# Kernel tuning notes

Hardware: AMD Instinct MI355X
Metric: run time of the kernel (lower is better)

The kernel has to match this reference:

```python
import jax, jax.numpy as jnp
import numpy as np

B, S, D = 2, 2048, 2048
H, KVH = 16, 4
HD = D // H  # 128


def _rope_angles(seq, head_dim):
    theta = 1.0 / (10000.0 ** (jnp.arange(0, head_dim, 2, dtype=jnp.float32) / head_dim))
    ang = jnp.arange(seq, dtype=jnp.float32)[:, None] * theta[None, :]  # [S, HD/2]
    return jnp.cos(ang), jnp.sin(ang)


def _apply_rotary(t, cos, sin):
    # t: [B, S, h, HD]; pairs are (even, odd) along last dim (view_as_complex semantics)
    tr = t[..., 0::2]
    ti = t[..., 1::2]
    c = cos[None, :, None, :]
    s = sin[None, :, None, :]
    out_r = tr * c - ti * s
    out_i = tr * s + ti * c
    return jnp.stack([out_r, out_i], axis=-1).reshape(t.shape)


def setup_inputs() -> dict:
    key = jax.random.key(0)
    ks = jax.random.split(key, 8)
    sd = 1.0 / np.sqrt(D)
    return {
        'x': jax.random.normal(ks[0], (B, S, D), dtype=jnp.float32),
        'wq': jax.random.normal(ks[1], (D, D), dtype=jnp.float32) * sd,
        'bq': jax.random.normal(ks[2], (D,), dtype=jnp.float32) * 0.01,
        'wk': jax.random.normal(ks[3], (D, KVH * HD), dtype=jnp.float32) * sd,
        'bk': jax.random.normal(ks[4], (KVH * HD,), dtype=jnp.float32) * 0.01,
        'wv': jax.random.normal(ks[5], (D, KVH * HD), dtype=jnp.float32) * sd,
        'bv': jax.random.normal(ks[6], (KVH * HD,), dtype=jnp.float32) * 0.01,
        'wo': jax.random.normal(ks[7], (D, D), dtype=jnp.float32) * sd,
    }


def reference(x, wq, bq, wk, bk, wv, bv, wo):
    b, s, d = x.shape
    q = (x @ wq + bq).reshape(b, s, H, HD)
    k = (x @ wk + bk).reshape(b, s, KVH, HD)
    v = (x @ wv + bv).reshape(b, s, KVH, HD)

    cos, sin = _rope_angles(s, HD)
    q = _apply_rotary(q, cos, sin)
    k = _apply_rotary(k, cos, sin)

    repeat = H // KVH
    k = jnp.repeat(k, repeat, axis=2)  # [B, S, H, HD]
    v = jnp.repeat(v, repeat, axis=2)

    scale = 1.0 / np.sqrt(HD)
    att_score = jnp.einsum('bqhd,bkhd->bqhk', q, k) * scale  # [B, S, H, S]
    att_weight = jax.nn.softmax(att_score, axis=-1)
    out = jnp.einsum('bqhk,bkhd->bqhd', att_weight, v)
    out = out.reshape(b, s, H * HD)
    return out @ wo
```

## Files before the change

kernel.cpp:

```cpp
#include <hip/hip_runtime.h>
#include <hip/hip_bf16.h>
#include <cstdint>

typedef __attribute__((ext_vector_type(4))) float f32x4;
typedef __attribute__((ext_vector_type(16))) float f32x16;
typedef __attribute__((ext_vector_type(8))) short bf16x8;
typedef __attribute__((ext_vector_type(4))) unsigned int u32x4;
typedef unsigned short u16;
typedef unsigned int u32;

__device__ __forceinline__ u16 f2b(float x) {
  __hip_bfloat16 h = __float2bfloat16(x);
  return *reinterpret_cast<u16*>(&h);
}

__device__ __forceinline__ u32 pk(float a, float b) {
  return ((u32)f2b(b) << 16) | (u32)f2b(a);
}

__device__ __forceinline__ void gload16(const void* g, void* l) {
  __builtin_amdgcn_global_load_lds((const __attribute__((address_space(1))) u32*)g,
                                   (__attribute__((address_space(3))) u32*)l, 16, 0, 0);
}

__device__ __forceinline__ float xmax32(float x) {
  return fmaxf(x, __shfl_xor(x, 32, 64));
}
__device__ __forceinline__ float xsum32(float x) {
  return x + __shfl_xor(x, 32, 64);
}


__global__ void cvt_f32_bf16(const float* __restrict__ in, u16* __restrict__ out, int n4) {
  int idx = (blockIdx.x * 256 + threadIdx.x);
  if (idx < n4) {
    const float4 v = *(const float4*)(in + (size_t)idx * 4);
    u16* o = out + (size_t)idx * 4;
    o[0] = f2b(v.x); o[1] = f2b(v.y); o[2] = f2b(v.z); o[3] = f2b(v.w);
  }
}

__global__ void w_transpose_cvt(const float* __restrict__ w0, const float* __restrict__ w1,
                                const float* __restrict__ w2, int b0, int b1,
                                int N0, int N1, int N2,
                                u16* __restrict__ out, int K) {
  __shared__ float tile[32][33];
  int k0 = blockIdx.x * 32, n0 = blockIdx.y * 32;
  const float* src; int srcN; int c0;
  if (n0 < b0)      { src = w0; srcN = N0; c0 = n0; }
  else if (n0 < b1) { src = w1; srcN = N1; c0 = n0 - b0; }
  else              { src = w2; srcN = N2; c0 = n0 - b1; }
  int tx = threadIdx.x & 31, ty = threadIdx.x >> 5;
#pragma unroll
  for (int j = 0; j < 32; j += 8)
    tile[ty + j][tx] = src[(size_t)(k0 + ty + j) * srcN + c0 + tx];
  __syncthreads();
#pragma unroll
  for (int j = 0; j < 32; j += 8)
    out[(size_t)(n0 + ty + j) * K + k0 + tx] = f2b(tile[tx][ty + j]);
}

__global__ void pack_bias(const float* __restrict__ bq, const float* __restrict__ bk,
                          const float* __restrict__ bv, float* __restrict__ out) {
  int i = blockIdx.x * 256 + threadIdx.x;
  if (i < 3072) out[i] = (i < 2048) ? bq[i] : ((i < 2560) ? bk[i - 2048] : bv[i - 2560]);
}

__global__ void v_transpose_cvt(const float* __restrict__ qkv, u16* __restrict__ vt) {
  __shared__ float tile[32][33];
  int s0 = blockIdx.x * 32;
  int d0 = blockIdx.y * 32;
  int z = blockIdx.z;
  int b = z >> 2, kvh = z & 3;
  int tx = threadIdx.x & 31, ty = threadIdx.x >> 5;
#pragma unroll
  for (int j = 0; j < 32; j += 8)
    tile[ty + j][tx] = qkv[((size_t)(b * 2048 + s0 + ty + j)) * 3072 + 2560 + kvh * 128 + d0 + tx];
  __syncthreads();
#pragma unroll
  for (int j = 0; j < 32; j += 8)
    vt[((size_t)z * 128 + d0 + ty + j) * 2048 + s0 + tx] = f2b(tile[tx][ty + j]);
}

__global__ void rope_cvt(const float* __restrict__ qkv, u16* __restrict__ out,
                         int lognh, int col0, float scale) {
  int idx = blockIdx.x * 256 + threadIdx.x;
  int i = idx & 63;
  int nh = 1 << lognh;
  int h = (idx >> 6) & (nh - 1);
  int bs = idx >> (6 + lognh);
  int s = bs & 2047;
  int b = bs >> 11;
  const float* src = qkv + (size_t)bs * 3072 + col0 + h * 128 + 2 * i;
  float tr = src[0], ti = src[1];
  float theta = expf(-(float)i * 0.14391156831212787f);
  float ang = (float)s * theta;
  float sv, cv;
  sincosf(ang, &sv, &cv);
  float orr = (tr * cv - ti * sv) * scale;
  float oii = (tr * sv + ti * cv) * scale;
  u16* dst = out + (((size_t)(b * nh + h) * 2048 + s) * 128 + 2 * i);
  dst[0] = f2b(orr);
  dst[1] = f2b(oii);
}

__global__ __launch_bounds__(256) void gemm_bt_bf16(
    const u16* __restrict__ A, const u16* __restrict__ Bt,
    const float* __restrict__ bias, float* __restrict__ C,
    int M, int N, int K) {
  __shared__ u16 As[128 * 32];
  __shared__ u16 Bs[128 * 32];
  const int tid = threadIdx.x;
  const int lane = tid & 63;
  const int w = tid >> 6;
  const int wr = w >> 1, wc = w & 1;
  const int m0 = blockIdx.y * 128;
  const int n0 = blockIdx.x * 128;

  f32x4 acc[4][4] = {};

  for (int k0 = 0; k0 < K; k0 += 32) {
#pragma unroll
    for (int it = 0; it < 2; ++it) {
      int c = tid + it * 256;
      int row = c >> 2;
      int off = (c & 3) * 8;
      gload16(A + (size_t)(m0 + row) * K + k0 + off, (u16*)As + w * 512 + it * 2048);
      gload16(Bt + (size_t)(n0 + row) * K + k0 + off, (u16*)Bs + w * 512 + it * 2048);
    }
    __syncthreads();
    const int col8 = (lane >> 4) * 8;
    bf16x8 a[4], bfr[4];
#pragma unroll
    for (int m = 0; m < 4; ++m)
      a[m] = *(const bf16x8*)&As[(wr * 64 + m * 16 + (lane & 15)) * 32 + col8];
#pragma unroll
    for (int n = 0; n < 4; ++n)
      bfr[n] = *(const bf16x8*)&Bs[(wc * 64 + n * 16 + (lane & 15)) * 32 + col8];
#pragma unroll
    for (int m = 0; m < 4; ++m)
#pragma unroll
      for (int n = 0; n < 4; ++n)
        acc[m][n] = __builtin_amdgcn_mfma_f32_16x16x32_bf16(a[m], bfr[n], acc[m][n], 0, 0, 0);
    __syncthreads();
  }

#pragma unroll
  for (int m = 0; m < 4; ++m) {
    int row = m0 + wr * 64 + m * 16 + ((lane >> 4) << 2);
#pragma unroll
    for (int n = 0; n < 4; ++n) {
      int col = n0 + wc * 64 + n * 16 + (lane & 15);
      float bvv = bias ? bias[col] : 0.f;
      float* cp = C + (size_t)row * N + col;
#pragma unroll
      for (int r = 0; r < 4; ++r) cp[(size_t)r * N] = acc[m][n][r] + bvv;
    }
  }
}

__global__ __launch_bounds__(128, 3) void flash_attn(
    const u16* __restrict__ Qr, const u16* __restrict__ Kr,
    const u16* __restrict__ Vt, u16* __restrict__ Att) {
  __shared__ u16 Ks[2][32 * 128];
  __shared__ u16 Vs[2][128 * 32];
  const int tid = threadIdx.x, lane = tid & 63, w = tid >> 6;
  const int lo = lane & 31, hi = lane >> 5;
  const int q0 = blockIdx.x * 64 + w * 32;
  const int h = blockIdx.y, b = blockIdx.z;
  const int kvh = h >> 2;

  const char* Khead = (const char*)(Kr + (size_t)(b * 4 + kvh) * 2048 * 128);
  const char* Vhead = (const char*)(Vt + (size_t)(b * 4 + kvh) * 128 * 2048);

  bf16x8 qf[8];
  {
    const u16* qp = Qr + ((size_t)(b * 16 + h) * 2048 + q0 + lo) * 128 + hi * 8;
#pragma unroll
    for (int ds = 0; ds < 8; ++ds) qf[ds] = *(const bf16x8*)(qp + ds * 16);
  }

#define STAGE(bufi, t)                                                        \
  {                                                                           \
    _Pragma("unroll")                                                         \
    for (int it = 0; it < 4; ++it) {                                          \
      int c = it * 128 + tid;                                                 \
      int krow = c >> 4;                                                      \
      int koff = krow * 256 + ((c & 15) << 4 ^ ((krow & 7) << 4));            \
      gload16(Khead + (size_t)(t) * 8192 + koff,                              \
              (u16*)Ks[bufi] + it * 1024 + w * 512);                          \
      int vrow = c >> 2;                                                      \
      int voff = vrow * 4096 + ((c & 3) << 4 ^ (((vrow >> 1) & 3) << 4));     \
      gload16(Vhead + (size_t)(t) * 64 + voff,                                \
              (u16*)Vs[bufi] + it * 1024 + w * 512);                          \
    }                                                                         \
  }

  f32x16 o0 = {}, o1 = {}, o2 = {}, o3 = {};
  float m_run = -3.0e38f, l_run = 0.f;
  const int swz = (lo & 7) << 4;
  const int vswz = ((lo >> 1) & 3) << 4;
  const int hi16 = hi * 16;

  STAGE(0, 0);
  __syncthreads();

  int buf = 0;
  for (int t = 0; t < 64; ++t) {
    int tn = (t < 63) ? t + 1 : 63;
    STAGE(buf ^ 1, tn);

    const char* Kb = (const char*)Ks[buf];
    const char* Vb = (const char*)Vs[buf];

    f32x16 sc = {};
    __builtin_amdgcn_s_setprio(1);
#pragma unroll
    for (int ds = 0; ds < 8; ++ds) {
      bf16x8 kf = *(const bf16x8*)(Kb + lo * 256 + ((ds * 32 + hi16) ^ swz));
      sc = __builtin_amdgcn_mfma_f32_32x32x16_bf16(kf, qf[ds], sc, 0, 0, 0);
    }
    __builtin_amdgcn_s_setprio(0);

    float m01 = fmaxf(fmaxf(sc[0], sc[1]), fmaxf(sc[2], sc[3]));
    float m23 = fmaxf(fmaxf(sc[4], sc[5]), fmaxf(sc[6], sc[7]));
    float m45 = fmaxf(fmaxf(sc[8], sc[9]), fmaxf(sc[10], sc[11]));
    float m67 = fmaxf(fmaxf(sc[12], sc[13]), fmaxf(sc[14], sc[15]));
    float pmax = xmax32(fmaxf(fmaxf(m01, m23), fmaxf(m45, m67)));

    if (!__all(pmax - m_run <= 8.0f)) {
      float mnew = fmaxf(m_run, pmax);
      float rs = __expf(m_run - mnew);
      m_run = mnew;
      l_run *= rs;
#pragma unroll
      for (int r = 0; r < 16; ++r) {
        float rsr = __shfl(rs, (r & 3) + 8 * (r >> 2) + 4 * hi, 64);
        o0[r] *= rsr; o1[r] *= rsr; o2[r] *= rsr; o3[r] *= rsr;
      }
    }

    float lsum = 0.f;
#pragma unroll
    for (int r = 0; r < 16; ++r) { float p = __expf(sc[r] - m_run); sc[r] = p; lsum += p; }
    l_run += xsum32(lsum);

    bf16x8 pa0, pa1;
    {
      u32 a0 = pk(sc[0], sc[1]),   a1 = pk(sc[2], sc[3]);
      u32 b0 = pk(sc[4], sc[5]),   b1 = pk(sc[6], sc[7]);
      u32 t0 = hi ? a0 : b0, t1 = hi ? a1 : b1;
      u32 r0 = __shfl_xor(t0, 32, 64), r1 = __shfl_xor(t1, 32, 64);
      u32x4 w0;
      w0[0] = hi ? r0 : a0; w0[1] = hi ? r1 : a1;
      w0[2] = hi ? b0 : r0; w0[3] = hi ? b1 : r1;
      pa0 = __builtin_bit_cast(bf16x8, w0);
      u32 c0 = pk(sc[8], sc[9]),   c1 = pk(sc[10], sc[11]);
      u32 d0 = pk(sc[12], sc[13]), d1 = pk(sc[14], sc[15]);
      u32 t2 = hi ? c0 : d0, t3 = hi ? c1 : d1;
      u32 r2 = __shfl_xor(t2, 32, 64), r3 = __shfl_xor(t3, 32, 64);
      u32x4 w1;
      w1[0] = hi ? r2 : c0; w1[1] = hi ? r3 : c1;
      w1[2] = hi ? d0 : r2; w1[3] = hi ? d1 : r3;
      pa1 = __builtin_bit_cast(bf16x8, w1);
    }

    __builtin_amdgcn_s_setprio(1);
#define PVN(on, n)                                                                                     \
    {                                                                                                  \
      const char* vrb = Vb + ((n) * 32 + lo) * 64;                                                     \
      on = __builtin_amdgcn_mfma_f32_32x32x16_bf16(pa0, *(const bf16x8*)(vrb + ((0  + hi16) ^ vswz)), on, 0, 0, 0); \
      on = __builtin_amdgcn_mfma_f32_32x32x16_bf16(pa1, *(const bf16x8*)(vrb + ((32 + hi16) ^ vswz)), on, 0, 0, 0); \
    }
    PVN(o0, 0)
    PVN(o1, 1)
    PVN(o2, 2)
    PVN(o3, 3)
    __builtin_amdgcn_s_setprio(0);

    __syncthreads();
    buf ^= 1;
  }

  float inv = 1.0f / l_run;
  size_t rowbase = (size_t)(b * 2048 + q0);
#pragma unroll
  for (int r = 0; r < 16; ++r) {
    int rr = (r & 3) + 8 * (r >> 2) + 4 * hi;
    float invr = __shfl(inv, rr, 64);
    u16* op = Att + (rowbase + rr) * 2048 + h * 128 + lo;
    op[0]  = f2b(o0[r] * invr);
    op[32] = f2b(o1[r] * invr);
    op[64] = f2b(o2[r] * invr);
    op[96] = f2b(o3[r] * invr);
  }
}


extern "C" void kernel_launch(void* const* d_in, const int* in_sizes, int n_in,
                              void* d_out, int out_size, void* d_ws, size_t ws_size,
                              hipStream_t stream) {
  const float* x  = (const float*)d_in[0];
  const float* wq = (const float*)d_in[1];
  const float* bq = (const float*)d_in[2];
  const float* wk = (const float*)d_in[3];
  const float* bk = (const float*)d_in[4];
  const float* wv = (const float*)d_in[5];
  const float* bv = (const float*)d_in[6];
  const float* wo = (const float*)d_in[7];
  float* out = (float*)d_out;
  char* ws = (char*)d_ws;

  u16*   x_bf   = (u16*)  (ws + 0);
  u16*   att    = (u16*)  (ws + 0);
  u16*   wqkv_t = (u16*)  (ws + 16777216);
  u16*   wo_t   = (u16*)  (ws + 29360128);
  float* biasq  = (float*)(ws + 37748736);
  float* qkv    = (float*)(ws + 37761024);
  u16*   q_r    = (u16*)  (ws + 88092672);
  u16*   k_r    = (u16*)  (ws + 104869888);
  u16*   v_t    = (u16*)  (ws + 109064192);

  cvt_f32_bf16<<<8192, 256, 0, stream>>>(x, x_bf, 2097152);
  w_transpose_cvt<<<dim3(64, 96), 256, 0, stream>>>(wq, wk, wv, 2048, 2560,
                                                    2048, 512, 512, wqkv_t, 2048);
  w_transpose_cvt<<<dim3(64, 64), 256, 0, stream>>>(wo, wo, wo, 2048, 2560,
                                                    2048, 2048, 2048, wo_t, 2048);
  pack_bias<<<12, 256, 0, stream>>>(bq, bk, bv, biasq);

  gemm_bt_bf16<<<dim3(24, 32), 256, 0, stream>>>(x_bf, wqkv_t, biasq, qkv, 4096, 3072, 2048);

  rope_cvt<<<16384, 256, 0, stream>>>(qkv, q_r, 4, 0, 0.08838834764831845f);
  rope_cvt<<<4096, 256, 0, stream>>>(qkv, k_r, 2, 2048, 1.0f);
  v_transpose_cvt<<<dim3(64, 4, 8), 256, 0, stream>>>(qkv, v_t);

  flash_attn<<<dim3(32, 16, 2), 128, 0, stream>>>(q_r, k_r, v_t, att);

  gemm_bt_bf16<<<dim3(16, 32), 256, 0, stream>>>(att, wo_t, nullptr, out, 4096, 2048, 2048);
}
```

Measured before the change: 294.6 us.

## Process two 32-row query tiles per wave in flash attention

Each wave now handles 64 query rows (two 32-row sub-tiles) instead of 32. Every K and V fragment read from LDS feeds two MFMAs, and each staged K/V tile is shared by twice as many queries. The grid is halved to 512 blocks and launch bounds drop to one block per SIMD, so register pressure rises and fewer waves are available to hide latency. This may reduce occupancy and latency hiding on a 256-CU device.

```diff
diff --git a/kernel.cpp b/kernel.cpp
--- a/kernel.cpp
+++ b/kernel.cpp
@@ -159,25 +159,28 @@
   }
 }
 
-__global__ __launch_bounds__(128, 3) void flash_attn(
+__global__ __launch_bounds__(128, 1) void flash_attn(
     const u16* __restrict__ Qr, const u16* __restrict__ Kr,
     const u16* __restrict__ Vt, u16* __restrict__ Att) {
   __shared__ u16 Ks[2][32 * 128];
   __shared__ u16 Vs[2][128 * 32];
   const int tid = threadIdx.x, lane = tid & 63, w = tid >> 6;
   const int lo = lane & 31, hi = lane >> 5;
-  const int q0 = blockIdx.x * 64 + w * 32;
+  const int q0 = blockIdx.x * 128 + w * 64;
   const int h = blockIdx.y, b = blockIdx.z;
   const int kvh = h >> 2;
 
   const char* Khead = (const char*)(Kr + (size_t)(b * 4 + kvh) * 2048 * 128);
   const char* Vhead = (const char*)(Vt + (size_t)(b * 4 + kvh) * 128 * 2048);
 
-  bf16x8 qf[8];
+  bf16x8 qf0[8], qf1[8];
   {
     const u16* qp = Qr + ((size_t)(b * 16 + h) * 2048 + q0 + lo) * 128 + hi * 8;
 #pragma unroll
-    for (int ds = 0; ds < 8; ++ds) qf[ds] = *(const bf16x8*)(qp + ds * 16);
+    for (int ds = 0; ds < 8; ++ds) qf0[ds] = *(const bf16x8*)(qp + ds * 16);
+    qp += (size_t)32 * 128;
+#pragma unroll
+    for (int ds = 0; ds < 8; ++ds) qf1[ds] = *(const bf16x8*)(qp + ds * 16);
   }
 
 #define STAGE(bufi, t)                                                        \
@@ -196,8 +199,9 @@
     }                                                                         \
   }
 
-  f32x16 o0 = {}, o1 = {}, o2 = {}, o3 = {};
-  float m_run = -3.0e38f, l_run = 0.f;
+  f32x16 o0[4] = {}, o1[4] = {};
+  float m_run0 = -3.0e38f, l_run0 = 0.f;
+  float m_run1 = -3.0e38f, l_run1 = 0.f;
   const int swz = (lo & 7) << 4;
   const int vswz = ((lo >> 1) & 3) << 4;
   const int hi16 = hi * 16;
@@ -213,86 +217,96 @@
     const char* Kb = (const char*)Ks[buf];
     const char* Vb = (const char*)Vs[buf];
 
-    f32x16 sc = {};
+    f32x16 s0 = {}, s1 = {};
     __builtin_amdgcn_s_setprio(1);
 #pragma unroll
     for (int ds = 0; ds < 8; ++ds) {
       bf16x8 kf = *(const bf16x8*)(Kb + lo * 256 + ((ds * 32 + hi16) ^ swz));
-      sc = __builtin_amdgcn_mfma_f32_32x32x16_bf16(kf, qf[ds], sc, 0, 0, 0);
+      s0 = __builtin_amdgcn_mfma_f32_32x32x16_bf16(kf, qf0[ds], s0, 0, 0, 0);
+      s1 = __builtin_amdgcn_mfma_f32_32x32x16_bf16(kf, qf1[ds], s1, 0, 0, 0);
     }
     __builtin_amdgcn_s_setprio(0);
 
-    float m01 = fmaxf(fmaxf(sc[0], sc[1]), fmaxf(sc[2], sc[3]));
-    float m23 = fmaxf(fmaxf(sc[4], sc[5]), fmaxf(sc[6], sc[7]));
-    float m45 = fmaxf(fmaxf(sc[8], sc[9]), fmaxf(sc[10], sc[11]));
-    float m67 = fmaxf(fmaxf(sc[12], sc[13]), fmaxf(sc[14], sc[15]));
-    float pmax = xmax32(fmaxf(fmaxf(m01, m23), fmaxf(m45, m67)));
-
-    if (!__all(pmax - m_run <= 8.0f)) {
-      float mnew = fmaxf(m_run, pmax);
-      float rs = __expf(m_run - mnew);
-      m_run = mnew;
-      l_run *= rs;
-#pragma unroll
-      for (int r = 0; r < 16; ++r) {
-        float rsr = __shfl(rs, (r & 3) + 8 * (r >> 2) + 4 * hi, 64);
-        o0[r] *= rsr; o1[r] *= rsr; o2[r] *= rsr; o3[r] *= rsr;
-      }
-    }
-
-    float lsum = 0.f;
-#pragma unroll
-    for (int r = 0; r < 16; ++r) { float p = __expf(sc[r] - m_run); sc[r] = p; lsum += p; }
-    l_run += xsum32(lsum);
-
-    bf16x8 pa0, pa1;
-    {
-      u32 a0 = pk(sc[0], sc[1]),   a1 = pk(sc[2], sc[3]);
-      u32 b0 = pk(sc[4], sc[5]),   b1 = pk(sc[6], sc[7]);
-      u32 t0 = hi ? a0 : b0, t1 = hi ? a1 : b1;
-      u32 r0 = __shfl_xor(t0, 32, 64), r1 = __shfl_xor(t1, 32, 64);
-      u32x4 w0;
-      w0[0] = hi ? r0 : a0; w0[1] = hi ? r1 : a1;
-      w0[2] = hi ? b0 : r0; w0[3] = hi ? b1 : r1;
-      pa0 = __builtin_bit_cast(bf16x8, w0);
-      u32 c0 = pk(sc[8], sc[9]),   c1 = pk(sc[10], sc[11]);
-      u32 d0 = pk(sc[12], sc[13]), d1 = pk(sc[14], sc[15]);
-      u32 t2 = hi ? c0 : d0, t3 = hi ? c1 : d1;
-      u32 r2 = __shfl_xor(t2, 32, 64), r3 = __shfl_xor(t3, 32, 64);
-      u32x4 w1;
-      w1[0] = hi ? r2 : c0; w1[1] = hi ? r3 : c1;
-      w1[2] = hi ? d0 : r2; w1[3] = hi ? d1 : r3;
-      pa1 = __builtin_bit_cast(bf16x8, w1);
-    }
+    bf16x8 paA0, paB0, paA1, paB1;
+#define SOFTPASS(S, MR, LR, OA, PA, PB)                                       \
+    {                                                                         \
+      float m01 = fmaxf(fmaxf(S[0], S[1]), fmaxf(S[2], S[3]));                \
+      float m23 = fmaxf(fmaxf(S[4], S[5]), fmaxf(S[6], S[7]));                \
+      float m45 = fmaxf(fmaxf(S[8], S[9]), fmaxf(S[10], S[11]));              \
+      float m67 = fmaxf(fmaxf(S[12], S[13]), fmaxf(S[14], S[15]));            \
+      float pmax = xmax32(fmaxf(fmaxf(m01, m23), fmaxf(m45, m67)));           \
+      if (!__all(pmax - MR <= 8.0f)) {                                        \
+        float mnew = fmaxf(MR, pmax);                                         \
+        float rs = __expf(MR - mnew);                                         \
+        MR = mnew;                                                            \
+        LR *= rs;                                                             \
+        _Pragma("unroll")                                                     \
+        for (int r = 0; r < 16; ++r) {                                        \
+          float rsr = __shfl(rs, (r & 3) + 8 * (r >> 2) + 4 * hi, 64);        \
+          OA[0][r] *= rsr; OA[1][r] *= rsr; OA[2][r] *= rsr; OA[3][r] *= rsr; \
+        }                                                                     \
+      }                                                                       \
+      float lsum = 0.f;                                                       \
+      _Pragma("unroll")                                                       \
+      for (int r = 0; r < 16; ++r) {                                          \
+        float p = __expf(S[r] - MR); S[r] = p; lsum += p;                     \
+      }                                                                       \
+      LR += xsum32(lsum);                                                     \
+      u32 a0 = pk(S[0], S[1]),   a1 = pk(S[2], S[3]);                         \
+      u32 b0 = pk(S[4], S[5]),   b1 = pk(S[6], S[7]);                         \
+      u32 t0 = hi ? a0 : b0, t1 = hi ? a1 : b1;                               \
+      u32 r0 = __shfl_xor(t0, 32, 64), r1 = __shfl_xor(t1, 32, 64);           \
+      u32x4 w0;                                                               \
+      w0[0] = hi ? r0 : a0; w0[1] = hi ? r1 : a1;                             \
+      w0[2] = hi ? b0 : r0; w0[3] = hi ? b1 : r1;                             \
+      PA = __builtin_bit_cast(bf16x8, w0);                                    \
+      u32 c0 = pk(S[8], S[9]),   c1 = pk(S[10], S[11]);                       \
+      u32 d0 = pk(S[12], S[13]), d1 = pk(S[14], S[15]);                       \
+      u32 t2 = hi ? c0 : d0, t3 = hi ? c1 : d1;                               \
+      u32 r2 = __shfl_xor(t2, 32, 64), r3 = __shfl_xor(t3, 32, 64);           \
+      u32x4 w1;                                                               \
+      w1[0] = hi ? r2 : c0; w1[1] = hi ? r3 : c1;                             \
+      w1[2] = hi ? d0 : r2; w1[3] = hi ? d1 : r3;                             \
+      PB = __builtin_bit_cast(bf16x8, w1);                                    \
+    }
+    SOFTPASS(s0, m_run0, l_run0, o0, paA0, paB0)
+    SOFTPASS(s1, m_run1, l_run1, o1, paA1, paB1)
 
     __builtin_amdgcn_s_setprio(1);
-#define PVN(on, n)                                                                                     \
-    {                                                                                                  \
-      const char* vrb = Vb + ((n) * 32 + lo) * 64;                                                     \
-      on = __builtin_amdgcn_mfma_f32_32x32x16_bf16(pa0, *(const bf16x8*)(vrb + ((0  + hi16) ^ vswz)), on, 0, 0, 0); \
-      on = __builtin_amdgcn_mfma_f32_32x32x16_bf16(pa1, *(const bf16x8*)(vrb + ((32 + hi16) ^ vswz)), on, 0, 0, 0); \
-    }
-    PVN(o0, 0)
-    PVN(o1, 1)
-    PVN(o2, 2)
-    PVN(o3, 3)
+#pragma unroll
+    for (int n = 0; n < 4; ++n) {
+      const char* vrb = Vb + (n * 32 + lo) * 64;
+      bf16x8 vb0 = *(const bf16x8*)(vrb + ((0  + hi16) ^ vswz));
+      bf16x8 vb1 = *(const bf16x8*)(vrb + ((32 + hi16) ^ vswz));
+      o0[n] = __builtin_amdgcn_mfma_f32_32x32x16_bf16(paA0, vb0, o0[n], 0, 0, 0);
+      o0[n] = __builtin_amdgcn_mfma_f32_32x32x16_bf16(paB0, vb1, o0[n], 0, 0, 0);
+      o1[n] = __builtin_amdgcn_mfma_f32_32x32x16_bf16(paA1, vb0, o1[n], 0, 0, 0);
+      o1[n] = __builtin_amdgcn_mfma_f32_32x32x16_bf16(paB1, vb1, o1[n], 0, 0, 0);
+    }
     __builtin_amdgcn_s_setprio(0);
 
     __syncthreads();
     buf ^= 1;
   }
 
-  float inv = 1.0f / l_run;
+  float inv0 = 1.0f / l_run0;
+  float inv1 = 1.0f / l_run1;
   size_t rowbase = (size_t)(b * 2048 + q0);
 #pragma unroll
   for (int r = 0; r < 16; ++r) {
     int rr = (r & 3) + 8 * (r >> 2) + 4 * hi;
-    float invr = __shfl(inv, rr, 64);
-    u16* op = Att + (rowbase + rr) * 2048 + h * 128 + lo;
-    op[0]  = f2b(o0[r] * invr);
-    op[32] = f2b(o1[r] * invr);
-    op[64] = f2b(o2[r] * invr);
-    op[96] = f2b(o3[r] * invr);
+    float iv0 = __shfl(inv0, rr, 64);
+    float iv1 = __shfl(inv1, rr, 64);
+    u16* op0 = Att + (rowbase + rr) * 2048 + h * 128 + lo;
+    u16* op1 = Att + (rowbase + 32 + rr) * 2048 + h * 128 + lo;
+    op0[0]  = f2b(o0[0][r] * iv0);
+    op0[32] = f2b(o0[1][r] * iv0);
+    op0[64] = f2b(o0[2][r] * iv0);
+    op0[96] = f2b(o0[3][r] * iv0);
+    op1[0]  = f2b(o1[0][r] * iv1);
+    op1[32] = f2b(o1[1][r] * iv1);
+    op1[64] = f2b(o1[2][r] * iv1);
+    op1[96] = f2b(o1[3][r] * iv1);
   }
 }
 
@@ -334,7 +348,7 @@
   rope_cvt<<<4096, 256, 0, stream>>>(qkv, k_r, 2, 2048, 1.0f);
   v_transpose_cvt<<<dim3(64, 4, 8), 256, 0, stream>>>(qkv, v_t);
 
-  flash_attn<<<dim3(32, 16, 2), 128, 0, stream>>>(q_r, k_r, v_t, att);
+  flash_attn<<<dim3(16, 16, 2), 128, 0, stream>>>(q_r, k_r, v_t, att);
 
   gemm_bt_bf16<<<dim3(16, 32), 256, 0, stream>>>(att, wo_t, nullptr, out, 4096, 2048, 2048);
 }
```

New measurement: 303.1 us. +2.9%, slower.

## Store QKV projection as bf16 and swizzle GEMM block order across XCDs

Applied to the files above, without the earlier changes.

The QKV GEMM now writes bf16 instead of fp32, which halves the intermediate buffer traffic. The rope and V-transpose kernels now read that bf16 buffer, and rope uses packed 32-bit loads and stores. Both GEMMs switch to a 1D grid whose block index is remapped so that consecutive tiles land on the same XCD, aiming for better L2 reuse. The change also rounds the pre-RoPE values to bf16, which adds a small precision loss.

```diff
diff --git a/kernel.cpp b/kernel.cpp
--- a/kernel.cpp
+++ b/kernel.cpp
@@ -14,8 +14,14 @@
   return *reinterpret_cast<u16*>(&h);
 }
 
+__device__ __forceinline__ float b2f(u32 u) {
+  u32 v = u << 16;
+  return __builtin_bit_cast(float, v);
+}
+
 __device__ __forceinline__ u32 pk(float a, float b) {
-  return ((u32)f2b(b) << 16) | (u32)f2b(a);
+  __hip_bfloat162 h2 = __float22bfloat162_rn(float2{a, b});
+  return *reinterpret_cast<u32*>(&h2);
 }
 
 __device__ __forceinline__ void gload16(const void* g, void* l) {
@@ -66,8 +72,8 @@
   if (i < 3072) out[i] = (i < 2048) ? bq[i] : ((i < 2560) ? bk[i - 2048] : bv[i - 2560]);
 }
 
-__global__ void v_transpose_cvt(const float* __restrict__ qkv, u16* __restrict__ vt) {
-  __shared__ float tile[32][33];
+__global__ void v_transpose_cvt(const u16* __restrict__ qkv, u16* __restrict__ vt) {
+  __shared__ u16 tile[32][34];
   int s0 = blockIdx.x * 32;
   int d0 = blockIdx.y * 32;
   int z = blockIdx.z;
@@ -79,10 +85,10 @@
   __syncthreads();
 #pragma unroll
   for (int j = 0; j < 32; j += 8)
-    vt[((size_t)z * 128 + d0 + ty + j) * 2048 + s0 + tx] = f2b(tile[tx][ty + j]);
-}
-
-__global__ void rope_cvt(const float* __restrict__ qkv, u16* __restrict__ out,
+    vt[((size_t)z * 128 + d0 + ty + j) * 2048 + s0 + tx] = tile[tx][ty + j];
+}
+
+__global__ void rope_cvt(const u16* __restrict__ qkv, u16* __restrict__ out,
                          int lognh, int col0, float scale) {
   int idx = blockIdx.x * 256 + threadIdx.x;
   int i = idx & 63;
@@ -91,31 +97,31 @@
   int bs = idx >> (6 + lognh);
   int s = bs & 2047;
   int b = bs >> 11;
-  const float* src = qkv + (size_t)bs * 3072 + col0 + h * 128 + 2 * i;
-  float tr = src[0], ti = src[1];
+  u32 pr = *(const u32*)(qkv + (size_t)bs * 3072 + col0 + h * 128 + 2 * i);
+  float tr = b2f(pr & 0xffffu), ti = b2f(pr >> 16);
   float theta = expf(-(float)i * 0.14391156831212787f);
   float ang = (float)s * theta;
   float sv, cv;
   sincosf(ang, &sv, &cv);
   float orr = (tr * cv - ti * sv) * scale;
   float oii = (tr * sv + ti * cv) * scale;
-  u16* dst = out + (((size_t)(b * nh + h) * 2048 + s) * 128 + 2 * i);
-  dst[0] = f2b(orr);
-  dst[1] = f2b(oii);
+  *(u32*)(out + (((size_t)(b * nh + h) * 2048 + s) * 128 + 2 * i)) = pk(orr, oii);
 }
 
 __global__ __launch_bounds__(256) void gemm_bt_bf16(
     const u16* __restrict__ A, const u16* __restrict__ Bt,
-    const float* __restrict__ bias, float* __restrict__ C,
-    int M, int N, int K) {
+    const float* __restrict__ bias, void* __restrict__ Cv,
+    int M, int N, int K, int gx, int obf16) {
   __shared__ u16 As[128 * 32];
   __shared__ u16 Bs[128 * 32];
   const int tid = threadIdx.x;
   const int lane = tid & 63;
   const int w = tid >> 6;
   const int wr = w >> 1, wc = w & 1;
-  const int m0 = blockIdx.y * 128;
-  const int n0 = blockIdx.x * 128;
+  const int nb = gridDim.x;
+  const int swz = (blockIdx.x & 7) * (nb >> 3) + (blockIdx.x >> 3);
+  const int m0 = (swz / gx) * 128;
+  const int n0 = (swz % gx) * 128;
 
   f32x4 acc[4][4] = {};
 
@@ -152,9 +158,15 @@
     for (int n = 0; n < 4; ++n) {
       int col = n0 + wc * 64 + n * 16 + (lane & 15);
       float bvv = bias ? bias[col] : 0.f;
-      float* cp = C + (size_t)row * N + col;
-#pragma unroll
-      for (int r = 0; r < 4; ++r) cp[(size_t)r * N] = acc[m][n][r] + bvv;
+      if (obf16) {
+        u16* cp = (u16*)Cv + (size_t)row * N + col;
+#pragma unroll
+        for (int r = 0; r < 4; ++r) cp[(size_t)r * N] = f2b(acc[m][n][r] + bvv);
+      } else {
+        float* cp = (float*)Cv + (size_t)row * N + col;
+#pragma unroll
+        for (int r = 0; r < 4; ++r) cp[(size_t)r * N] = acc[m][n][r] + bvv;
+      }
     }
   }
 }
@@ -316,7 +328,7 @@
   u16*   wqkv_t = (u16*)  (ws + 16777216);
   u16*   wo_t   = (u16*)  (ws + 29360128);
   float* biasq  = (float*)(ws + 37748736);
-  float* qkv    = (float*)(ws + 37761024);
+  u16*   qkv    = (u16*)  (ws + 37761024);
   u16*   q_r    = (u16*)  (ws + 88092672);
   u16*   k_r    = (u16*)  (ws + 104869888);
   u16*   v_t    = (u16*)  (ws + 109064192);
@@ -328,7 +340,7 @@
                                                     2048, 2048, 2048, wo_t, 2048);
   pack_bias<<<12, 256, 0, stream>>>(bq, bk, bv, biasq);
 
-  gemm_bt_bf16<<<dim3(24, 32), 256, 0, stream>>>(x_bf, wqkv_t, biasq, qkv, 4096, 3072, 2048);
+  gemm_bt_bf16<<<768, 256, 0, stream>>>(x_bf, wqkv_t, biasq, qkv, 4096, 3072, 2048, 24, 1);
 
   rope_cvt<<<16384, 256, 0, stream>>>(qkv, q_r, 4, 0, 0.08838834764831845f);
   rope_cvt<<<4096, 256, 0, stream>>>(qkv, k_r, 2, 2048, 1.0f);
@@ -336,5 +348,5 @@
 
   flash_attn<<<dim3(32, 16, 2), 128, 0, stream>>>(q_r, k_r, v_t, att);
 
-  gemm_bt_bf16<<<dim3(16, 32), 256, 0, stream>>>(att, wo_t, nullptr, out, 4096, 2048, 2048);
-}
+  gemm_bt_bf16<<<512, 256, 0, stream>>>(att, wo_t, nullptr, out, 4096, 2048, 2048, 16, 0);
+}
```

New measurement: 292.0 us. About the same (-0.9%).
